# Kernel optimization log

Hardware: AMD Instinct MI355X
Metric: run time of the kernel (lower is better)

The kernel has to match this reference:

```python
import jax, jax.numpy as jnp
import numpy as np

B, S, M, H = 4, 512, 128, 768
KEY_SIZE, VALUE_SIZE = 30000, 10000


def setup_inputs() -> dict:
    key = jax.random.key(0)
    k1, k2, k3, k4, k5, k6 = jax.random.split(key, 6)
    return {
        "word_seq": jax.random.randint(k1, (B, M), 0, KEY_SIZE),
        "hidden_state": jax.random.normal(k2, (B, S, H), dtype=jnp.float32),
        "label_value_matrix": jax.random.randint(k3, (B, S, M), 0, VALUE_SIZE),
        "word_mask_metrix": jax.random.uniform(k4, (B, S, M), dtype=jnp.float32),
        "key_table": jax.random.normal(k5, (KEY_SIZE, H), dtype=jnp.float32) * 0.02,
        "value_table": jax.random.normal(k6, (VALUE_SIZE, H), dtype=jnp.float32) * 0.02,
    }


def reference(word_seq, hidden_state, label_value_matrix, word_mask_metrix,
              key_table, value_table):
    temper = jnp.asarray(H, hidden_state.dtype) ** 0.5
    emb_a = key_table[word_seq]                      # [B, M, H]
    # u[b,s,m] = <hidden_state[b,s], emb_a[b,m]> / sqrt(H)
    u = jnp.einsum('bsh,bmh->bsm', hidden_state, emb_a) / temper
    mask = jnp.clip(word_mask_metrix, 0.0, 1.0)      # [B, S, M]
    delta_exp_u = jnp.exp(u) * mask                  # masked unnormalized attn
    p = delta_exp_u / (jnp.sum(delta_exp_u, axis=2, keepdims=True) + 1e-10)
    emb_c = value_table[label_value_matrix]          # [B, S, M, H]
    # o[b,s,h] = sum_m p[b,s,m] * emb_c[b,s,m,h]
    o = jnp.einsum('bsm,bsmh->bsh', p, emb_c)
    return o
```

## Files before the change

### kernel.cpp

```cpp
#include <hip/hip_runtime.h>
#include <hip/hip_bf16.h>


constexpr int B = 4, S = 512, M = 128, H = 768;
constexpr int C4 = H / 4;
constexpr int KEY_SIZE = 30000, VALUE_SIZE = 10000;

constexpr int    VT_N      = VALUE_SIZE * H;
constexpr int    KA_N      = B * M * H;
constexpr size_t VT_BYTES  = (size_t)VT_N * 2;
constexpr size_t WS_NEEDED = VT_BYTES + (size_t)KA_N * 2;
constexpr int    VT_V4     = VT_N / 4;
constexpr int    KA_V4     = KA_N / 4;
constexpr int    CONV_TOTAL = VT_V4 + KA_V4;

__device__ inline unsigned short f2bf(float f) {
    __hip_bfloat16 h = __float2bfloat16(f);
    return *reinterpret_cast<unsigned short*>(&h);
}
__device__ inline float bf2f(unsigned short u) {
    return __uint_as_float((unsigned)u << 16);
}
__device__ inline float4 bf4_to_f4(ushort4 u) {
    float4 f;
    f.x = bf2f(u.x); f.y = bf2f(u.y); f.z = bf2f(u.z); f.w = bf2f(u.w);
    return f;
}

__global__ __launch_bounds__(256) void convert_kernel(
    const float* __restrict__ vt, const float* __restrict__ kt,
    const int* __restrict__ wseq,
    unsigned short* __restrict__ vt_bf, unsigned short* __restrict__ ka_bf)
{
    int i = blockIdx.x * 256 + threadIdx.x;
    if (i < VT_V4) {
        float4 f = ((const float4*)vt)[i];
        ushort4 u; u.x = f2bf(f.x); u.y = f2bf(f.y); u.z = f2bf(f.z); u.w = f2bf(f.w);
        ((ushort4*)vt_bf)[i] = u;
    } else if (i < CONV_TOTAL) {
        int j   = i - VT_V4;
        int c   = j % (H / 4);
        int row = j / (H / 4);
        int src = wseq[row];
        float4 f = ((const float4*)(kt + (size_t)src * H))[c];
        ushort4 u; u.x = f2bf(f.x); u.y = f2bf(f.y); u.z = f2bf(f.z); u.w = f2bf(f.w);
        ((ushort4*)ka_bf)[j] = u;
    }
}

__global__ __launch_bounds__(192) void kvmn_bf16_kernel(
    const float* __restrict__ hidden_state,
    const int*   __restrict__ lvm,
    const float* __restrict__ mask,
    const unsigned short* __restrict__ ka_bf,
    const unsigned short* __restrict__ vt_bf,
    float*       __restrict__ out)
{
    const int bs   = blockIdx.x;
    const int b    = bs / S;
    const int t    = threadIdx.x;
    const int lane = t & 63;
    const int wave = t >> 6;

    __shared__ float4 hs4_s[C4];
    __shared__ int    row_s[M];
    __shared__ float  mask_s[M];
    __shared__ float4 obuf[3][C4];
    __shared__ float  dsum_s[3];

    const float4* hs_g4 = (const float4*)(hidden_state + (size_t)bs * H);
    hs4_s[t] = hs_g4[t];
    if (t < M) {
        row_s[t]  = lvm[(size_t)bs * M + t];
        float mk  = mask[(size_t)bs * M + t];
        mask_s[t] = fminf(fmaxf(mk, 0.f), 1.f);
    }
    __syncthreads();

    const float4 h0 = hs4_s[lane];
    const float4 h1 = hs4_s[lane + 64];
    const float4 h2 = hs4_s[lane + 128];

    const float inv_temper = rsqrtf((float)H);

    float4 a0 = {0.f, 0.f, 0.f, 0.f};
    float4 a1 = {0.f, 0.f, 0.f, 0.f};
    float4 a2 = {0.f, 0.f, 0.f, 0.f};
    float  dsum = 0.f;

    #pragma unroll 4
    for (int m = wave; m < M; m += 3) {
        const ushort4* kr = (const ushort4*)(ka_bf + ((size_t)(b * M + m)) * H);
        const ushort4* vr = (const ushort4*)(vt_bf + (size_t)row_s[m] * H);
        const ushort4 ku0 = kr[lane];
        const ushort4 ku1 = kr[lane + 64];
        const ushort4 ku2 = kr[lane + 128];
        const ushort4 vu0 = vr[lane];
        const ushort4 vu1 = vr[lane + 64];
        const ushort4 vu2 = vr[lane + 128];

        const float4 k0 = bf4_to_f4(ku0);
        const float4 k1 = bf4_to_f4(ku1);
        const float4 k2 = bf4_to_f4(ku2);

        float dot = h0.x*k0.x + h0.y*k0.y + h0.z*k0.z + h0.w*k0.w
                  + h1.x*k1.x + h1.y*k1.y + h1.z*k1.z + h1.w*k1.w
                  + h2.x*k2.x + h2.y*k2.y + h2.z*k2.z + h2.w*k2.w;
        #pragma unroll
        for (int off = 1; off < 64; off <<= 1) dot += __shfl_xor(dot, off);

        const float delta = __expf(dot * inv_temper) * mask_s[m];
        dsum += delta;

        const float4 v0 = bf4_to_f4(vu0);
        const float4 v1 = bf4_to_f4(vu1);
        const float4 v2 = bf4_to_f4(vu2);
        a0.x += delta*v0.x; a0.y += delta*v0.y; a0.z += delta*v0.z; a0.w += delta*v0.w;
        a1.x += delta*v1.x; a1.y += delta*v1.y; a1.z += delta*v1.z; a1.w += delta*v1.w;
        a2.x += delta*v2.x; a2.y += delta*v2.y; a2.z += delta*v2.z; a2.w += delta*v2.w;
    }

    obuf[wave][lane]       = a0;
    obuf[wave][lane + 64]  = a1;
    obuf[wave][lane + 128] = a2;
    if (lane == 0) dsum_s[wave] = dsum;
    __syncthreads();

    const float inv_d = 1.0f / (dsum_s[0] + dsum_s[1] + dsum_s[2] + 1e-10f);
    const float4 r0 = obuf[0][t];
    const float4 r1 = obuf[1][t];
    const float4 r2 = obuf[2][t];
    float4 r;
    r.x = (r0.x + r1.x + r2.x) * inv_d;
    r.y = (r0.y + r1.y + r2.y) * inv_d;
    r.z = (r0.z + r1.z + r2.z) * inv_d;
    r.w = (r0.w + r1.w + r2.w) * inv_d;
    ((float4*)(out + (size_t)bs * H))[t] = r;
}

__global__ __launch_bounds__(192) void kvmn_fp32_kernel(
    const int*   __restrict__ word_seq,
    const float* __restrict__ hidden_state,
    const int*   __restrict__ lvm,
    const float* __restrict__ mask,
    const float* __restrict__ key_table,
    const float* __restrict__ value_table,
    float*       __restrict__ out)
{
    const int bs   = blockIdx.x;
    const int b    = bs / S;
    const int t    = threadIdx.x;
    const int lane = t & 63;
    const int wave = t >> 6;

    __shared__ float4 hs4_s[C4];
    __shared__ int    wseq_s[M];
    __shared__ int    row_s[M];
    __shared__ float  mask_s[M];
    __shared__ float4 obuf[3][C4];
    __shared__ float  dsum_s[3];

    const float4* hs_g4 = (const float4*)(hidden_state + (size_t)bs * H);
    hs4_s[t] = hs_g4[t];
    if (t < M) {
        wseq_s[t] = word_seq[b * M + t];
        row_s[t]  = lvm[(size_t)bs * M + t];
        float mk  = mask[(size_t)bs * M + t];
        mask_s[t] = fminf(fmaxf(mk, 0.f), 1.f);
    }
    __syncthreads();

    const float4 h0 = hs4_s[lane];
    const float4 h1 = hs4_s[lane + 64];
    const float4 h2 = hs4_s[lane + 128];
    const float inv_temper = rsqrtf((float)H);
    const float4* kt4 = (const float4*)key_table;
    const float4* vt4 = (const float4*)value_table;

    float4 a0 = {0.f,0.f,0.f,0.f}, a1 = {0.f,0.f,0.f,0.f}, a2 = {0.f,0.f,0.f,0.f};
    float dsum = 0.f;

    #pragma unroll 2
    for (int m = wave; m < M; m += 3) {
        const float4* kr = kt4 + (size_t)wseq_s[m] * C4;
        const float4* vr = vt4 + (size_t)row_s[m]  * C4;
        const float4 k0 = kr[lane], k1 = kr[lane+64], k2 = kr[lane+128];
        const float4 v0 = vr[lane], v1 = vr[lane+64], v2 = vr[lane+128];
        float dot = h0.x*k0.x + h0.y*k0.y + h0.z*k0.z + h0.w*k0.w
                  + h1.x*k1.x + h1.y*k1.y + h1.z*k1.z + h1.w*k1.w
                  + h2.x*k2.x + h2.y*k2.y + h2.z*k2.z + h2.w*k2.w;
        #pragma unroll
        for (int off = 1; off < 64; off <<= 1) dot += __shfl_xor(dot, off);
        const float delta = __expf(dot * inv_temper) * mask_s[m];
        dsum += delta;
        a0.x += delta*v0.x; a0.y += delta*v0.y; a0.z += delta*v0.z; a0.w += delta*v0.w;
        a1.x += delta*v1.x; a1.y += delta*v1.y; a1.z += delta*v1.z; a1.w += delta*v1.w;
        a2.x += delta*v2.x; a2.y += delta*v2.y; a2.z += delta*v2.z; a2.w += delta*v2.w;
    }
    obuf[wave][lane] = a0; obuf[wave][lane+64] = a1; obuf[wave][lane+128] = a2;
    if (lane == 0) dsum_s[wave] = dsum;
    __syncthreads();
    const float inv_d = 1.0f / (dsum_s[0] + dsum_s[1] + dsum_s[2] + 1e-10f);
    const float4 r0 = obuf[0][t], r1 = obuf[1][t], r2 = obuf[2][t];
    float4 r;
    r.x = (r0.x+r1.x+r2.x)*inv_d; r.y = (r0.y+r1.y+r2.y)*inv_d;
    r.z = (r0.z+r1.z+r2.z)*inv_d; r.w = (r0.w+r1.w+r2.w)*inv_d;
    ((float4*)(out + (size_t)bs * H))[t] = r;
}

extern "C" void kernel_launch(void* const* d_in, const int* in_sizes, int n_in,
                              void* d_out, int out_size, void* d_ws, size_t ws_size,
                              hipStream_t stream) {
    const int*   word_seq    = (const int*)  d_in[0];
    const float* hidden      = (const float*)d_in[1];
    const int*   lvm         = (const int*)  d_in[2];
    const float* mask        = (const float*)d_in[3];
    const float* key_table   = (const float*)d_in[4];
    const float* value_table = (const float*)d_in[5];
    float* out = (float*)d_out;

    if (ws_size >= WS_NEEDED) {
        unsigned short* vt_bf = (unsigned short*)d_ws;
        unsigned short* ka_bf = (unsigned short*)((char*)d_ws + VT_BYTES);
        convert_kernel<<<(CONV_TOTAL + 255) / 256, 256, 0, stream>>>(
            value_table, key_table, word_seq, vt_bf, ka_bf);
        kvmn_bf16_kernel<<<B * S, 192, 0, stream>>>(
            hidden, lvm, mask, ka_bf, vt_bf, out);
    } else {
        kvmn_fp32_kernel<<<B * S, 192, 0, stream>>>(
            word_seq, hidden, lvm, mask, key_table, value_table, out);
    }
}
```

Measured before the change: 212.2 us.

## Split attention scores into MFMA bf16 GEMM phase and separate value-gather kernel

Computes the query-key scores u for all (b,s,m) up front with a batched bf16 MFMA GEMM kernel (16x16x32 tiles) instead of per-row dot products with wave shuffle reductions inside the gather loop. Hidden states are now also converted to bf16 in the convert kernel, and the scores are written to a float workspace. The gather kernel then reads precomputed scores, applies exp and the mask once per m, and accumulates value rows using 6 waves instead of 3. This removes the key reads and shuffle reductions from the gather loop, at the cost of an extra kernel launch, extra workspace traffic, and bf16 rounding of the hidden state.

New measurement: 206.3 us. -2.8%, faster.

```diff
diff --git a/kernel.cpp b/kernel.cpp
--- a/kernel.cpp
+++ b/kernel.cpp
@@ -6,13 +6,22 @@
 constexpr int C4 = H / 4;
 constexpr int KEY_SIZE = 30000, VALUE_SIZE = 10000;
 
-constexpr int    VT_N      = VALUE_SIZE * H;
-constexpr int    KA_N      = B * M * H;
-constexpr size_t VT_BYTES  = (size_t)VT_N * 2;
-constexpr size_t WS_NEEDED = VT_BYTES + (size_t)KA_N * 2;
-constexpr int    VT_V4     = VT_N / 4;
-constexpr int    KA_V4     = KA_N / 4;
-constexpr int    CONV_TOTAL = VT_V4 + KA_V4;
+constexpr int VT_N = VALUE_SIZE * H;
+constexpr int KA_N = B * M * H;
+constexpr int HS_N = B * S * H;
+constexpr int U_N  = B * S * M;
+
+constexpr size_t VT_BYTES = (size_t)VT_N * 2;
+constexpr size_t KA_BYTES = (size_t)KA_N * 2;
+constexpr size_t HS_BYTES = (size_t)HS_N * 2;
+constexpr size_t U_BYTES  = (size_t)U_N  * 4;
+constexpr size_t WS_NEEDED = VT_BYTES + KA_BYTES + HS_BYTES + U_BYTES;
+
+constexpr int VT_V4 = VT_N / 4, KA_V4 = KA_N / 4, HS_V4 = HS_N / 4;
+constexpr int CONV_TOTAL = VT_V4 + KA_V4 + HS_V4;
+
+typedef short  bf16x8  __attribute__((ext_vector_type(8)));
+typedef float  floatx4 __attribute__((ext_vector_type(4)));
 
 __device__ inline unsigned short f2bf(float f) {
     __hip_bfloat16 h = __float2bfloat16(f);
@@ -26,98 +35,110 @@
     f.x = bf2f(u.x); f.y = bf2f(u.y); f.z = bf2f(u.z); f.w = bf2f(u.w);
     return f;
 }
+__device__ inline ushort4 f4_to_bf4(float4 f) {
+    ushort4 u; u.x = f2bf(f.x); u.y = f2bf(f.y); u.z = f2bf(f.z); u.w = f2bf(f.w);
+    return u;
+}
 
 __global__ __launch_bounds__(256) void convert_kernel(
     const float* __restrict__ vt, const float* __restrict__ kt,
-    const int* __restrict__ wseq,
-    unsigned short* __restrict__ vt_bf, unsigned short* __restrict__ ka_bf)
+    const float* __restrict__ hs, const int* __restrict__ wseq,
+    unsigned short* __restrict__ vt_bf, unsigned short* __restrict__ ka_bf,
+    unsigned short* __restrict__ hs_bf)
 {
     int i = blockIdx.x * 256 + threadIdx.x;
     if (i < VT_V4) {
-        float4 f = ((const float4*)vt)[i];
-        ushort4 u; u.x = f2bf(f.x); u.y = f2bf(f.y); u.z = f2bf(f.z); u.w = f2bf(f.w);
-        ((ushort4*)vt_bf)[i] = u;
-    } else if (i < CONV_TOTAL) {
+        ((ushort4*)vt_bf)[i] = f4_to_bf4(((const float4*)vt)[i]);
+    } else if (i < VT_V4 + KA_V4) {
         int j   = i - VT_V4;
         int c   = j % (H / 4);
         int row = j / (H / 4);
         int src = wseq[row];
         float4 f = ((const float4*)(kt + (size_t)src * H))[c];
-        ushort4 u; u.x = f2bf(f.x); u.y = f2bf(f.y); u.z = f2bf(f.z); u.w = f2bf(f.w);
-        ((ushort4*)ka_bf)[j] = u;
-    }
-}
-
-__global__ __launch_bounds__(192) void kvmn_bf16_kernel(
-    const float* __restrict__ hidden_state,
+        ((ushort4*)ka_bf)[j] = f4_to_bf4(f);
+    } else if (i < CONV_TOTAL) {
+        int j = i - VT_V4 - KA_V4;
+        ((ushort4*)hs_bf)[j] = f4_to_bf4(((const float4*)hs)[j]);
+    }
+}
+
+__global__ __launch_bounds__(256) void phaseA_kernel(
+    const unsigned short* __restrict__ hs_bf,
+    const unsigned short* __restrict__ ka_bf,
+    float* __restrict__ u_ws)
+{
+    const int lane = threadIdx.x & 63;
+    const int wave = threadIdx.x >> 6;
+    const int tile = blockIdx.x * 4 + wave;
+    const int b    = tile >> 8;
+    const int r    = tile & 255;
+    const int s0   = (r >> 3) << 4;
+    const int m0   = (r & 7) << 4;
+    const int l15  = lane & 15;
+    const int quad = lane >> 4;
+
+    const unsigned short* arow = hs_bf + (size_t)(b * S + s0 + l15) * H + quad * 8;
+    const unsigned short* brow = ka_bf + (size_t)(b * M + m0 + l15) * H + quad * 8;
+
+    floatx4 acc = {0.f, 0.f, 0.f, 0.f};
+    #pragma unroll 4
+    for (int k = 0; k < H; k += 32) {
+        bf16x8 af = *(const bf16x8*)(arow + k);
+        bf16x8 bf = *(const bf16x8*)(brow + k);
+        acc = __builtin_amdgcn_mfma_f32_16x16x32_bf16(af, bf, acc, 0, 0, 0);
+    }
+    float* up = u_ws + (size_t)(b * S + s0 + quad * 4) * M + m0 + l15;
+    up[0 * M] = acc[0];
+    up[1 * M] = acc[1];
+    up[2 * M] = acc[2];
+    up[3 * M] = acc[3];
+}
+
+constexpr int GW = 6;
+__global__ __launch_bounds__(384) void gather_kernel(
+    const float* __restrict__ u_ws,
     const int*   __restrict__ lvm,
     const float* __restrict__ mask,
-    const unsigned short* __restrict__ ka_bf,
     const unsigned short* __restrict__ vt_bf,
     float*       __restrict__ out)
 {
     const int bs   = blockIdx.x;
-    const int b    = bs / S;
     const int t    = threadIdx.x;
     const int lane = t & 63;
     const int wave = t >> 6;
 
-    __shared__ float4 hs4_s[C4];
+    __shared__ float  delta_s[M];
     __shared__ int    row_s[M];
-    __shared__ float  mask_s[M];
-    __shared__ float4 obuf[3][C4];
-    __shared__ float  dsum_s[3];
-
-    const float4* hs_g4 = (const float4*)(hidden_state + (size_t)bs * H);
-    hs4_s[t] = hs_g4[t];
+    __shared__ float4 obuf[GW][C4];
+    __shared__ float  dsum_s[GW];
+
+    const float inv_temper = rsqrtf((float)H);
     if (t < M) {
-        row_s[t]  = lvm[(size_t)bs * M + t];
-        float mk  = mask[(size_t)bs * M + t];
-        mask_s[t] = fminf(fmaxf(mk, 0.f), 1.f);
-    }
-    __syncthreads();
-
-    const float4 h0 = hs4_s[lane];
-    const float4 h1 = hs4_s[lane + 64];
-    const float4 h2 = hs4_s[lane + 128];
-
-    const float inv_temper = rsqrtf((float)H);
-
-    float4 a0 = {0.f, 0.f, 0.f, 0.f};
-    float4 a1 = {0.f, 0.f, 0.f, 0.f};
-    float4 a2 = {0.f, 0.f, 0.f, 0.f};
-    float  dsum = 0.f;
+        float u  = u_ws[(size_t)bs * M + t];
+        float mk = mask[(size_t)bs * M + t];
+        mk = fminf(fmaxf(mk, 0.f), 1.f);
+        delta_s[t] = __expf(u * inv_temper) * mk;
+        row_s[t]   = lvm[(size_t)bs * M + t];
+    }
+    __syncthreads();
+
+    float4 a0 = {0.f,0.f,0.f,0.f}, a1 = {0.f,0.f,0.f,0.f}, a2 = {0.f,0.f,0.f,0.f};
+    float dsum = 0.f;
 
     #pragma unroll 4
-    for (int m = wave; m < M; m += 3) {
-        const ushort4* kr = (const ushort4*)(ka_bf + ((size_t)(b * M + m)) * H);
+    for (int m = wave; m < M; m += GW) {
+        const float pm = delta_s[m];
         const ushort4* vr = (const ushort4*)(vt_bf + (size_t)row_s[m] * H);
-        const ushort4 ku0 = kr[lane];
-        const ushort4 ku1 = kr[lane + 64];
-        const ushort4 ku2 = kr[lane + 128];
         const ushort4 vu0 = vr[lane];
         const ushort4 vu1 = vr[lane + 64];
         const ushort4 vu2 = vr[lane + 128];
-
-        const float4 k0 = bf4_to_f4(ku0);
-        const float4 k1 = bf4_to_f4(ku1);
-        const float4 k2 = bf4_to_f4(ku2);
-
-        float dot = h0.x*k0.x + h0.y*k0.y + h0.z*k0.z + h0.w*k0.w
-                  + h1.x*k1.x + h1.y*k1.y + h1.z*k1.z + h1.w*k1.w
-                  + h2.x*k2.x + h2.y*k2.y + h2.z*k2.z + h2.w*k2.w;
-        #pragma unroll
-        for (int off = 1; off < 64; off <<= 1) dot += __shfl_xor(dot, off);
-
-        const float delta = __expf(dot * inv_temper) * mask_s[m];
-        dsum += delta;
-
+        dsum += pm;
         const float4 v0 = bf4_to_f4(vu0);
         const float4 v1 = bf4_to_f4(vu1);
         const float4 v2 = bf4_to_f4(vu2);
-        a0.x += delta*v0.x; a0.y += delta*v0.y; a0.z += delta*v0.z; a0.w += delta*v0.w;
-        a1.x += delta*v1.x; a1.y += delta*v1.y; a1.z += delta*v1.z; a1.w += delta*v1.w;
-        a2.x += delta*v2.x; a2.y += delta*v2.y; a2.z += delta*v2.z; a2.w += delta*v2.w;
+        a0.x += pm*v0.x; a0.y += pm*v0.y; a0.z += pm*v0.z; a0.w += pm*v0.w;
+        a1.x += pm*v1.x; a1.y += pm*v1.y; a1.z += pm*v1.z; a1.w += pm*v1.w;
+        a2.x += pm*v2.x; a2.y += pm*v2.y; a2.z += pm*v2.z; a2.w += pm*v2.w;
     }
 
     obuf[wave][lane]       = a0;
@@ -126,16 +147,20 @@
     if (lane == 0) dsum_s[wave] = dsum;
     __syncthreads();
 
-    const float inv_d = 1.0f / (dsum_s[0] + dsum_s[1] + dsum_s[2] + 1e-10f);
-    const float4 r0 = obuf[0][t];
-    const float4 r1 = obuf[1][t];
-    const float4 r2 = obuf[2][t];
-    float4 r;
-    r.x = (r0.x + r1.x + r2.x) * inv_d;
-    r.y = (r0.y + r1.y + r2.y) * inv_d;
-    r.z = (r0.z + r1.z + r2.z) * inv_d;
-    r.w = (r0.w + r1.w + r2.w) * inv_d;
-    ((float4*)(out + (size_t)bs * H))[t] = r;
+    if (t < C4) {
+        float d = 1e-10f;
+        #pragma unroll
+        for (int w = 0; w < GW; ++w) d += dsum_s[w];
+        const float inv_d = 1.0f / d;
+        float4 r = {0.f, 0.f, 0.f, 0.f};
+        #pragma unroll
+        for (int w = 0; w < GW; ++w) {
+            const float4 o = obuf[w][t];
+            r.x += o.x; r.y += o.y; r.z += o.z; r.w += o.w;
+        }
+        r.x *= inv_d; r.y *= inv_d; r.z *= inv_d; r.w *= inv_d;
+        ((float4*)(out + (size_t)bs * H))[t] = r;
+    }
 }
 
 __global__ __launch_bounds__(192) void kvmn_fp32_kernel(
@@ -222,10 +247,15 @@
     if (ws_size >= WS_NEEDED) {
         unsigned short* vt_bf = (unsigned short*)d_ws;
         unsigned short* ka_bf = (unsigned short*)((char*)d_ws + VT_BYTES);
+        unsigned short* hs_bf = (unsigned short*)((char*)d_ws + VT_BYTES + KA_BYTES);
+        float*          u_ws  = (float*)((char*)d_ws + VT_BYTES + KA_BYTES + HS_BYTES);
+
         convert_kernel<<<(CONV_TOTAL + 255) / 256, 256, 0, stream>>>(
-            value_table, key_table, word_seq, vt_bf, ka_bf);
-        kvmn_bf16_kernel<<<B * S, 192, 0, stream>>>(
-            hidden, lvm, mask, ka_bf, vt_bf, out);
+            value_table, key_table, hidden, word_seq, vt_bf, ka_bf, hs_bf);
+        phaseA_kernel<<<(B * S / 16) * (M / 16) / 4, 256, 0, stream>>>(
+            hs_bf, ka_bf, u_ws);
+        gather_kernel<<<B * S, 64 * GW, 0, stream>>>(
+            u_ws, lvm, mask, vt_bf, out);
     } else {
         kvmn_fp32_kernel<<<B * S, 192, 0, stream>>>(
             word_seq, hidden, lvm, mask, key_table, value_table, out);
```
